# Optimization experiments

Measured on AMD Instinct MI355X. Metric: run time of the kernel, lower is better.

## Reference

```python
import jax, jax.numpy as jnp
import numpy as np


def setup_inputs() -> dict:
    key = jax.random.key(0)
    k1, k2, k3 = jax.random.split(key, 3)
    B, C, S, D = 8, 256, 2048, 64
    a = jax.random.normal(k1, (B, C, S), dtype=jnp.float32)
    b = jax.random.normal(k2, (B, S, D), dtype=jnp.float32)
    c = jax.random.normal(k3, (B, S, D), dtype=jnp.float32)
    return {"a": a, "b": b, "c": c}


def reference(a, b, c):
    # mid[b, n, m] = softmax_m(b @ c^T), unscaled
    scores = jnp.einsum("bnd,bmd->bnm", b, c)
    mid = jax.nn.softmax(scores, axis=-1)  # [B, S, S]
    # out = a @ mid^T + a  -> [B, C, S]
    out = jnp.einsum("bcm,bnm->bcn", a, mid) + a
    return out
```

## Files before the change

kernel.cpp:

```cpp
#include <hip/hip_runtime.h>
#include <stdint.h>

#define S 2048
#define DHEAD 64
#define CDIM 256
#define NBATCH 8
#define NMT 16

typedef __attribute__((ext_vector_type(4))) float f32x4;
typedef __attribute__((ext_vector_type(8))) short s16x8;
typedef __attribute__((ext_vector_type(8))) _Float16 f16x8;
typedef __attribute__((ext_vector_type(4))) unsigned short u16x4;

static __device__ __forceinline__ unsigned short f2bf(float f) {
    unsigned int u = __builtin_bit_cast(unsigned int, f);
    unsigned int r = (u + 0x7FFFu + ((u >> 16) & 1u)) >> 16;
    return (unsigned short)r;
}
static __device__ __forceinline__ unsigned short f2h(float f) {
    _Float16 h = (_Float16)f;
    return __builtin_bit_cast(unsigned short, h);
}

__global__ __launch_bounds__(256) void cvt_a_kernel(const float* __restrict__ a,
                                                    unsigned short* __restrict__ a16,
                                                    int n4) {
    int i = blockIdx.x * 256 + threadIdx.x;
    int stride = gridDim.x * 256;
    for (; i < n4; i += stride) {
        f32x4 v = ((const f32x4*)a)[i];
        u16x4 o;
        o.x = f2bf(v.x); o.y = f2bf(v.y); o.z = f2bf(v.z); o.w = f2bf(v.w);
        ((u16x4*)a16)[i] = o;
    }
}

__global__ __launch_bounds__(256) void scores_kernel(
    const float* __restrict__ Bq, const float* __restrict__ Ck,
    unsigned short* __restrict__ E, float* __restrict__ Lp, int b0, int nb)
{
    const int bid = blockIdx.x;
    int lb, idx;
    if (nb == 8) { lb = bid & 7; idx = bid >> 3; }
    else { lb = bid / (NMT * 16); idx = bid - lb * (NMT * 16); }
    const int gb = b0 + lb;
    const int mt = idx & 15;
    const int m0 = mt * 128;
    const int n0 = (idx >> 4) * 128;
    const float* __restrict__ bp = Bq + (size_t)gb * S * DHEAD;
    const float* __restrict__ cp = Ck + (size_t)gb * S * DHEAD;
    unsigned short* __restrict__ Ep = E + (size_t)lb * S * S;

    extern __shared__ char smem[];
    unsigned short* cs = (unsigned short*)smem;
    unsigned short* bs = cs + 128 * 72;
    unsigned short* es = (unsigned short*)smem;
    float* Lsh = (float*)(smem + 2 * 128 * 72 * 2);

    const int tid = threadIdx.x;
    const int lane = tid & 63;
    const int wid = tid >> 6;
    const int wr = wid >> 1, wc = wid & 1;
    const int q = lane >> 4, r15 = lane & 15;

    #pragma unroll
    for (int t = 0; t < 8; ++t) {
        int ch = tid + 256 * t;
        int row = ch >> 4, c4 = ch & 15;
        f32x4 cv = *(const f32x4*)&cp[(size_t)(m0 + row) * DHEAD + c4 * 4];
        f32x4 bv = *(const f32x4*)&bp[(size_t)(n0 + row) * DHEAD + c4 * 4];
        u16x4 co, bo;
        co.x = f2h(cv.x); co.y = f2h(cv.y); co.z = f2h(cv.z); co.w = f2h(cv.w);
        bo.x = f2h(bv.x); bo.y = f2h(bv.y); bo.z = f2h(bv.z); bo.w = f2h(bv.w);
        *(u16x4*)&cs[row * 72 + c4 * 4] = co;
        *(u16x4*)&bs[row * 72 + c4 * 4] = bo;
    }
    __syncthreads();

    f32x4 acc[4][4] = {};
    #pragma unroll
    for (int kk = 0; kk < 2; ++kk) {
        f16x8 af[4], bf[4];
        #pragma unroll
        for (int i = 0; i < 4; ++i)
            af[i] = *(const f16x8*)&cs[(wr * 64 + i * 16 + r15) * 72 + kk * 32 + q * 8];
        #pragma unroll
        for (int j = 0; j < 4; ++j)
            bf[j] = *(const f16x8*)&bs[(wc * 64 + j * 16 + r15) * 72 + kk * 32 + q * 8];
        #pragma unroll
        for (int i = 0; i < 4; ++i)
            #pragma unroll
            for (int j = 0; j < 4; ++j)
                acc[i][j] = __builtin_amdgcn_mfma_f32_16x16x32_f16(af[i], bf[j], acc[i][j], 0, 0, 0);
    }

    u16x4 pk[4][4];
    float sj[4] = {0.f, 0.f, 0.f, 0.f};
    #pragma unroll
    for (int i = 0; i < 4; ++i) {
        #pragma unroll
        for (int j = 0; j < 4; ++j) {
            float e0 = __expf(acc[i][j][0]);
            float e1 = __expf(acc[i][j][1]);
            float e2 = __expf(acc[i][j][2]);
            float e3 = __expf(acc[i][j][3]);
            pk[i][j].x = f2bf(e0); pk[i][j].y = f2bf(e1);
            pk[i][j].z = f2bf(e2); pk[i][j].w = f2bf(e3);
            sj[j] += (e0 + e1) + (e2 + e3);
        }
    }
    #pragma unroll
    for (int j = 0; j < 4; ++j) {
        sj[j] += __shfl_xor(sj[j], 16);
        sj[j] += __shfl_xor(sj[j], 32);
    }

    __syncthreads();

    #pragma unroll
    for (int i = 0; i < 4; ++i)
        #pragma unroll
        for (int j = 0; j < 4; ++j) {
            int nl = wc * 64 + j * 16 + r15;
            int ml = wr * 64 + i * 16 + q * 4;
            *(u16x4*)&es[nl * 136 + ml] = pk[i][j];
        }
    if (q == 0) {
        #pragma unroll
        for (int j = 0; j < 4; ++j)
            Lsh[wr * 128 + wc * 64 + j * 16 + r15] = sj[j];
    }
    __syncthreads();

    if (tid < 128)
        Lp[(size_t)lb * NMT * S + (size_t)mt * S + n0 + tid] = Lsh[tid] + Lsh[128 + tid];

    #pragma unroll
    for (int t = 0; t < 8; ++t) {
        int ch = tid + 256 * t;
        int row = ch >> 4, off = ch & 15;
        f32x4 v = *(const f32x4*)&es[row * 136 + off * 8];
        *(f32x4*)&Ep[(size_t)(n0 + row) * S + m0 + off * 8] = v;
    }
}

__global__ __launch_bounds__(256, 4) void gemm_kernel(
    const unsigned short* __restrict__ a16, const unsigned short* __restrict__ E,
    const float* __restrict__ Lp, const float* __restrict__ afull,
    float* __restrict__ out, int b0, int nb)
{
    const int bid = blockIdx.x;
    int lb, idx;
    if (nb == 8) { lb = bid & 7; idx = bid >> 3; }
    else { lb = bid / 64; idx = bid - lb * 64; }
    const int gb = b0 + lb;
    const int nt = idx >> 1, ct = idx & 1;
    const int n0 = nt * 64, c0 = ct * 128;

    const unsigned short* __restrict__ Ap = a16 + (size_t)gb * CDIM * S;
    const unsigned short* __restrict__ Bp = E + (size_t)lb * S * S;
    const float* __restrict__ ap = afull + (size_t)gb * CDIM * S;
    float* __restrict__ op = out + (size_t)gb * CDIM * S;

    __shared__ unsigned short As[128 * 72];
    __shared__ unsigned short Bs[64 * 72];

    const int tid = threadIdx.x;
    const int lane = tid & 63;
    const int w = tid >> 6;
    const int wr = w >> 1, wc = w & 1;
    const int q = lane >> 4, r15 = lane & 15;

    const int arow[4] = { (tid) >> 3, (tid + 256) >> 3, (tid + 512) >> 3, (tid + 768) >> 3 };
    const int aoff[4] = { (tid) & 7, (tid + 256) & 7, (tid + 512) & 7, (tid + 768) & 7 };
    const int brow[2] = { (tid) >> 3, (tid + 256) >> 3 };
    const int boff[2] = { (tid) & 7, (tid + 256) & 7 };

    f32x4 acc[4][2] = {};
    f32x4 avr[4], bvr[2];

    #pragma unroll
    for (int t = 0; t < 4; ++t)
        avr[t] = *(const f32x4*)&Ap[(size_t)(c0 + arow[t]) * S + aoff[t] * 8];
    #pragma unroll
    for (int t = 0; t < 2; ++t)
        bvr[t] = *(const f32x4*)&Bp[(size_t)(n0 + brow[t]) * S + boff[t] * 8];

    #pragma unroll 2
    for (int kt = 0; kt < S / 64; ++kt) {
        __syncthreads();
        #pragma unroll
        for (int t = 0; t < 4; ++t)
            *(f32x4*)&As[arow[t] * 72 + aoff[t] * 8] = avr[t];
        #pragma unroll
        for (int t = 0; t < 2; ++t)
            *(f32x4*)&Bs[brow[t] * 72 + boff[t] * 8] = bvr[t];
        __syncthreads();

        if (kt < S / 64 - 1) {
            const int k0n = (kt + 1) * 64;
            #pragma unroll
            for (int t = 0; t < 4; ++t)
                avr[t] = *(const f32x4*)&Ap[(size_t)(c0 + arow[t]) * S + k0n + aoff[t] * 8];
            #pragma unroll
            for (int t = 0; t < 2; ++t)
                bvr[t] = *(const f32x4*)&Bp[(size_t)(n0 + brow[t]) * S + k0n + boff[t] * 8];
        }

        #pragma unroll
        for (int kk = 0; kk < 2; ++kk) {
            s16x8 af[4], bf[2];
            #pragma unroll
            for (int i = 0; i < 4; ++i)
                af[i] = *(const s16x8*)&As[(wr * 64 + i * 16 + r15) * 72 + kk * 32 + q * 8];
            #pragma unroll
            for (int j = 0; j < 2; ++j)
                bf[j] = *(const s16x8*)&Bs[(wc * 32 + j * 16 + r15) * 72 + kk * 32 + q * 8];
            #pragma unroll
            for (int i = 0; i < 4; ++i)
                #pragma unroll
                for (int j = 0; j < 2; ++j)
                    acc[i][j] = __builtin_amdgcn_mfma_f32_16x16x32_bf16(af[i], bf[j], acc[i][j], 0, 0, 0);
        }
    }

    float rcpL[2];
    #pragma unroll
    for (int j = 0; j < 2; ++j) {
        int n = n0 + wc * 32 + j * 16 + r15;
        float s = 0.f;
        #pragma unroll
        for (int mt = 0; mt < NMT; ++mt)
            s += Lp[(size_t)lb * NMT * S + (size_t)mt * S + n];
        rcpL[j] = 1.0f / s;
    }
    #pragma unroll
    for (int i = 0; i < 4; ++i) {
        #pragma unroll
        for (int rr = 0; rr < 4; ++rr) {
            int cc = c0 + wr * 64 + i * 16 + q * 4 + rr;
            size_t base = (size_t)cc * S;
            #pragma unroll
            for (int j = 0; j < 2; ++j) {
                int n = n0 + wc * 32 + j * 16 + r15;
                op[base + n] = acc[i][j][rr] * rcpL[j] + ap[base + n];
            }
        }
    }
}

extern "C" void kernel_launch(void* const* d_in, const int* in_sizes, int n_in,
                              void* d_out, int out_size, void* d_ws, size_t ws_size,
                              hipStream_t stream) {
    const float* a = (const float*)d_in[0];
    const float* b = (const float*)d_in[1];
    const float* c = (const float*)d_in[2];
    float* out = (float*)d_out;

    const size_t a16_bytes = (size_t)NBATCH * CDIM * S * 2;
    const size_t perb = (size_t)S * S * 2 + (size_t)NMT * S * 4;
    int G = 1;
    if (ws_size > a16_bytes + perb) {
        size_t g = (ws_size - a16_bytes) / perb;
        G = (g >= NBATCH) ? NBATCH : (int)g;
        if (G < 1) G = 1;
    }
    unsigned short* a16 = (unsigned short*)d_ws;
    unsigned short* E = (unsigned short*)((char*)d_ws + a16_bytes);
    float* Lp = (float*)((char*)d_ws + a16_bytes + (size_t)G * S * S * 2);

    cvt_a_kernel<<<1024, 256, 0, stream>>>(a, a16, NBATCH * CDIM * S / 4);

    const size_t lds1 = 2 * 128 * 72 * 2 + 2 * 128 * 4;
    for (int b0 = 0; b0 < NBATCH; b0 += G) {
        int nb = (NBATCH - b0 < G) ? (NBATCH - b0) : G;
        scores_kernel<<<NMT * 16 * nb, 256, lds1, stream>>>(b, c, E, Lp, b0, nb);
        gemm_kernel<<<64 * nb, 256, 0, stream>>>(a16, E, Lp, a, out, b0, nb);
    }
}
```

Measured before the change: 62.92 us.

## Double-buffer LDS tiles in gemm and read residual from bf16 copy

The gemm kernel now keeps two LDS buffers for the A and E tiles. It writes the next tile into the alternate buffer after computing on the current one, which leaves one barrier per iteration instead of two. The residual term is now read from the bf16 converted copy of a instead of the fp32 input, which halves that epilogue read traffic. This lowers the residual's precision to bf16 and doubles LDS use per block, which may hurt occupancy at 4 blocks per CU.

```diff
diff --git a/kernel.cpp b/kernel.cpp
--- a/kernel.cpp
+++ b/kernel.cpp
@@ -20,6 +20,9 @@
 static __device__ __forceinline__ unsigned short f2h(float f) {
     _Float16 h = (_Float16)f;
     return __builtin_bit_cast(unsigned short, h);
+}
+static __device__ __forceinline__ float bf2f(unsigned short u) {
+    return __builtin_bit_cast(float, (unsigned int)u << 16);
 }
 
 __global__ __launch_bounds__(256) void cvt_a_kernel(const float* __restrict__ a,
@@ -146,8 +149,7 @@
 
 __global__ __launch_bounds__(256, 4) void gemm_kernel(
     const unsigned short* __restrict__ a16, const unsigned short* __restrict__ E,
-    const float* __restrict__ Lp, const float* __restrict__ afull,
-    float* __restrict__ out, int b0, int nb)
+    const float* __restrict__ Lp, float* __restrict__ out, int b0, int nb)
 {
     const int bid = blockIdx.x;
     int lb, idx;
@@ -159,11 +161,10 @@
 
     const unsigned short* __restrict__ Ap = a16 + (size_t)gb * CDIM * S;
     const unsigned short* __restrict__ Bp = E + (size_t)lb * S * S;
-    const float* __restrict__ ap = afull + (size_t)gb * CDIM * S;
     float* __restrict__ op = out + (size_t)gb * CDIM * S;
 
-    __shared__ unsigned short As[128 * 72];
-    __shared__ unsigned short Bs[64 * 72];
+    __shared__ unsigned short As[2][128 * 72];
+    __shared__ unsigned short Bs[2][64 * 72];
 
     const int tid = threadIdx.x;
     const int lane = tid & 63;
@@ -185,18 +186,17 @@
     #pragma unroll
     for (int t = 0; t < 2; ++t)
         bvr[t] = *(const f32x4*)&Bp[(size_t)(n0 + brow[t]) * S + boff[t] * 8];
+    #pragma unroll
+    for (int t = 0; t < 4; ++t)
+        *(f32x4*)&As[0][arow[t] * 72 + aoff[t] * 8] = avr[t];
+    #pragma unroll
+    for (int t = 0; t < 2; ++t)
+        *(f32x4*)&Bs[0][brow[t] * 72 + boff[t] * 8] = bvr[t];
+    __syncthreads();
 
     #pragma unroll 2
     for (int kt = 0; kt < S / 64; ++kt) {
-        __syncthreads();
-        #pragma unroll
-        for (int t = 0; t < 4; ++t)
-            *(f32x4*)&As[arow[t] * 72 + aoff[t] * 8] = avr[t];
-        #pragma unroll
-        for (int t = 0; t < 2; ++t)
-            *(f32x4*)&Bs[brow[t] * 72 + boff[t] * 8] = bvr[t];
-        __syncthreads();
-
+        const int cur = kt & 1;
         if (kt < S / 64 - 1) {
             const int k0n = (kt + 1) * 64;
             #pragma unroll
@@ -207,21 +207,35 @@
                 bvr[t] = *(const f32x4*)&Bp[(size_t)(n0 + brow[t]) * S + k0n + boff[t] * 8];
         }
 
+        const unsigned short* Ar = As[cur];
+        const unsigned short* Br = Bs[cur];
         #pragma unroll
         for (int kk = 0; kk < 2; ++kk) {
             s16x8 af[4], bf[2];
             #pragma unroll
             for (int i = 0; i < 4; ++i)
-                af[i] = *(const s16x8*)&As[(wr * 64 + i * 16 + r15) * 72 + kk * 32 + q * 8];
+                af[i] = *(const s16x8*)&Ar[(wr * 64 + i * 16 + r15) * 72 + kk * 32 + q * 8];
             #pragma unroll
             for (int j = 0; j < 2; ++j)
-                bf[j] = *(const s16x8*)&Bs[(wc * 32 + j * 16 + r15) * 72 + kk * 32 + q * 8];
+                bf[j] = *(const s16x8*)&Br[(wc * 32 + j * 16 + r15) * 72 + kk * 32 + q * 8];
             #pragma unroll
             for (int i = 0; i < 4; ++i)
                 #pragma unroll
                 for (int j = 0; j < 2; ++j)
                     acc[i][j] = __builtin_amdgcn_mfma_f32_16x16x32_bf16(af[i], bf[j], acc[i][j], 0, 0, 0);
         }
+
+        if (kt < S / 64 - 1) {
+            unsigned short* Aw = As[cur ^ 1];
+            unsigned short* Bw = Bs[cur ^ 1];
+            #pragma unroll
+            for (int t = 0; t < 4; ++t)
+                *(f32x4*)&Aw[arow[t] * 72 + aoff[t] * 8] = avr[t];
+            #pragma unroll
+            for (int t = 0; t < 2; ++t)
+                *(f32x4*)&Bw[brow[t] * 72 + boff[t] * 8] = bvr[t];
+        }
+        __syncthreads();
     }
 
     float rcpL[2];
@@ -243,7 +257,7 @@
             #pragma unroll
             for (int j = 0; j < 2; ++j) {
                 int n = n0 + wc * 32 + j * 16 + r15;
-                op[base + n] = acc[i][j][rr] * rcpL[j] + ap[base + n];
+                op[base + n] = acc[i][j][rr] * rcpL[j] + bf2f(Ap[base + n]);
             }
         }
     }
@@ -275,6 +289,6 @@
     for (int b0 = 0; b0 < NBATCH; b0 += G) {
         int nb = (NBATCH - b0 < G) ? (NBATCH - b0) : G;
         scores_kernel<<<NMT * 16 * nb, 256, lds1, stream>>>(b, c, E, Lp, b0, nb);
-        gemm_kernel<<<64 * nb, 256, 0, stream>>>(a16, E, Lp, a, out, b0, nb);
-    }
-}
+        gemm_kernel<<<64 * nb, 256, 0, stream>>>(a16, E, Lp, out, b0, nb);
+    }
+}
```

Measured after the change: 63.63 us. About the same (+1.1%).
